# Optimization experiments

Hardware: AMD Instinct MI355X
Metric: run time of the kernel (lower is better)

## Reference

```python
import jax, jax.numpy as jnp
import numpy as np

N_NODES = 50000
N_EDGES = 600000
NODE_DIM = 64
EDGE_DIM = 16
HIDDEN = 128
N_LAYERS = 3
N_CLASSES = 2
N_GRAPHS = 256
BN_EPS = 1e-5


def setup_inputs() -> dict:
    key = jax.random.key(0)
    ks = jax.random.split(key, 24)
    i = iter(range(24))
    def nrm(shape, scale=0.05):
        return jax.random.normal(ks[next(i)], shape, dtype=jnp.float32) * scale
    inp = {
        "x": jax.random.normal(ks[next(i)], (N_NODES, NODE_DIM), dtype=jnp.float32),
        "edge_index": jax.random.randint(ks[next(i)], (2, N_EDGES), 0, N_NODES),
        "edge_attr": jax.random.normal(ks[next(i)], (N_EDGES, EDGE_DIM), dtype=jnp.float32),
        "batch": jnp.sort(jax.random.randint(ks[next(i)], (N_NODES,), 0, N_GRAPHS)),
        # encoders
        "node_w": nrm((NODE_DIM, HIDDEN)), "node_b": jnp.zeros((HIDDEN,), jnp.float32),
        "edge_w": nrm((EDGE_DIM, HIDDEN)), "edge_b": jnp.zeros((HIDDEN,), jnp.float32),
        # per-layer GINE MLP params, stacked over layers
        "mlp_w1": nrm((N_LAYERS, HIDDEN, HIDDEN)), "mlp_b1": jnp.zeros((N_LAYERS, HIDDEN), jnp.float32),
        "mlp_w2": nrm((N_LAYERS, HIDDEN, HIDDEN)), "mlp_b2": jnp.zeros((N_LAYERS, HIDDEN), jnp.float32),
        "bn_gamma": jnp.ones((N_LAYERS, HIDDEN), jnp.float32), "bn_beta": jnp.zeros((N_LAYERS, HIDDEN), jnp.float32),
        # head
        "head_w1": nrm((HIDDEN, HIDDEN)), "head_b1": jnp.zeros((HIDDEN,), jnp.float32),
        "head_w2": nrm((HIDDEN, N_CLASSES)), "head_b2": jnp.zeros((N_CLASSES,), jnp.float32),
    }
    return inp


def _forward(x, edge_attr, node_w, node_b, edge_w, edge_b, mlp_w1, mlp_b1,
             mlp_w2, mlp_b2, bn_gamma, bn_beta, head_w1, head_b1, head_w2,
             head_b2, edge_index, batch):
    src, dst = edge_index[0], edge_index[1]
    h = x @ node_w + node_b                     # [N, H]
    ea = edge_attr @ edge_w + edge_b            # [E, H]
    for l in range(N_LAYERS):
        # GINE message: relu(x_src + edge_attr), scatter-add into dst
        msg = jax.nn.relu(h[src] + ea)          # [E, H]
        agg = jax.ops.segment_sum(msg, dst, num_segments=N_NODES)
        z = h + agg                              # (1+eps)*x + agg, eps=0
        z = jax.nn.relu(z @ mlp_w1[l] + mlp_b1[l]) @ mlp_w2[l] + mlp_b2[l]
        # BatchNorm1d over node dim (batch statistics)
        mean = jnp.mean(z, axis=0)
        var = jnp.var(z, axis=0)
        z = bn_gamma[l] * (z - mean) * jax.lax.rsqrt(var + BN_EPS) + bn_beta[l]
        h = jax.nn.relu(z)                       # dropout off (eval)
    g = jax.ops.segment_sum(h, batch, num_segments=N_GRAPHS)  # global_add_pool
    return jax.nn.relu(g @ head_w1 + head_b1) @ head_w2 + head_b2


def reference(x, edge_index, edge_attr, batch, node_w, node_b, edge_w, edge_b,
              mlp_w1, mlp_b1, mlp_w2, mlp_b2, bn_gamma, bn_beta,
              head_w1, head_b1, head_w2, head_b2):
    return _forward(x, edge_attr, node_w, node_b, edge_w, edge_b, mlp_w1,
                    mlp_b1, mlp_w2, mlp_b2, bn_gamma, bn_beta, head_w1,
                    head_b1, head_w2, head_b2, edge_index, batch)
```

## Files before the change

kernel.cpp:

```cpp
#include <hip/hip_runtime.h>

#define N_NODES_C 50000
#define N_EDGES_C 600000
#define NODE_DIM_C 64
#define EDGE_DIM_C 16
#define HID 128
#define N_GRAPHS_C 256
#define BN_EPS_C 1e-5f
#define SCAN_NBLK ((N_NODES_C + 255) / 256)

typedef short bf16x8 __attribute__((ext_vector_type(8)));
typedef float f32x4 __attribute__((ext_vector_type(4)));
typedef float f32x2 __attribute__((ext_vector_type(2)));

__device__ __forceinline__ unsigned short f2bf(float f) {
  union { float f; unsigned u; } v; v.f = f;
  unsigned r = (v.u + 0x7fffu + ((v.u >> 16) & 1u)) >> 16;
  return (unsigned short)r;
}

__device__ __forceinline__ float2 bfp2f(unsigned u) {
  union { unsigned u; float f; } lo, hi;
  lo.u = u << 16;
  hi.u = u & 0xffff0000u;
  return make_float2(lo.f, hi.f);
}

__device__ __forceinline__ float bf2f(unsigned short s) {
  union { unsigned u; float f; } v;
  v.u = ((unsigned)s) << 16;
  return v.f;
}

__device__ __forceinline__ float2 fp8p2f(unsigned short u) {
  f32x2 r = __builtin_amdgcn_cvt_pk_f32_fp8((int)(unsigned)u, false);
  return make_float2(r.x, r.y);
}

__global__ __launch_bounds__(256)
void k_x2bf(const float* __restrict__ x, unsigned short* __restrict__ xb,
            int* __restrict__ cnt, float* __restrict__ g) {
  int tid = blockIdx.x * 256 + threadIdx.x;
  size_t i = (size_t)tid * 4;
  if (i < (size_t)N_NODES_C * NODE_DIM_C) {
    float4 v = *(const float4*)&x[i];
    uint2 o;
    o.x = (unsigned)f2bf(v.x) | ((unsigned)f2bf(v.y) << 16);
    o.y = (unsigned)f2bf(v.z) | ((unsigned)f2bf(v.w) << 16);
    *(uint2*)&xb[i] = o;
  }
  if (tid < N_NODES_C) cnt[tid] = 0;
  if (tid < N_GRAPHS_C * HID) g[tid] = 0.f;
}

__global__ __launch_bounds__(256)
void k_prep_w(const float* __restrict__ w1, const float* __restrict__ w2,
              const float* __restrict__ nodew, unsigned short* __restrict__ wT) {
  int m = blockIdx.x;
  if (m < 6) {
    const float* src = (m < 3) ? (w1 + (size_t)m * HID * HID)
                               : (w2 + (size_t)(m - 3) * HID * HID);
    unsigned short* dst = wT + (size_t)m * HID * HID;
    for (int i = threadIdx.x; i < HID * HID; i += 256) {
      int n = i >> 7, k = i & 127;
      dst[n * HID + k] = f2bf(src[k * HID + n]);
    }
  } else {
    unsigned short* dst = wT + (size_t)6 * HID * HID;
    for (int i = threadIdx.x; i < HID * NODE_DIM_C; i += 256) {
      int n = i >> 6, k = i & 63;
      dst[n * NODE_DIM_C + k] = f2bf(nodew[k * HID + n]);
    }
  }
}

__global__ __launch_bounds__(256)
void k_node_mfma(const unsigned short* __restrict__ xb,
                 const unsigned short* __restrict__ nwT,
                 const float* __restrict__ bias, unsigned short* __restrict__ h) {
  const int LD = NODE_DIM_C + 8;
  __shared__ unsigned short a_lds[128 * LD];
  __shared__ unsigned short w_lds[128 * LD];
  int t = threadIdx.x;
  int row0 = blockIdx.x * 128;
  {
    int r = t >> 3, c = t & 7;
#pragma unroll
    for (int it = 0; it < 4; ++it) {
      int row = it * 32 + r;
      int grow = row0 + row;
      uint4 va = (grow < N_NODES_C)
                     ? ((const uint4*)(xb + (size_t)grow * NODE_DIM_C))[c]
                     : make_uint4(0, 0, 0, 0);
      *(uint4*)&a_lds[row * LD + c * 8] = va;
      uint4 vw = ((const uint4*)(nwT + (size_t)row * NODE_DIM_C))[c];
      *(uint4*)&w_lds[row * LD + c * 8] = vw;
    }
  }
  __syncthreads();

  int lane = t & 63;
  int w = t >> 6;
  int l15 = lane & 15;
  int q = lane >> 4;

  f32x4 acc[2][8];
#pragma unroll
  for (int rt = 0; rt < 2; ++rt)
#pragma unroll
    for (int nt = 0; nt < 8; ++nt) acc[rt][nt] = (f32x4)0.f;

#pragma unroll
  for (int kk = 0; kk < 2; ++kk) {
    int k0 = kk * 32;
    bf16x8 af[2];
#pragma unroll
    for (int rt = 0; rt < 2; ++rt) {
      int arow = w * 32 + rt * 16 + l15;
      af[rt] = *(const bf16x8*)&a_lds[arow * LD + k0 + q * 8];
    }
#pragma unroll
    for (int nt = 0; nt < 8; ++nt) {
      bf16x8 bf = *(const bf16x8*)&w_lds[(nt * 16 + l15) * LD + k0 + q * 8];
#pragma unroll
      for (int rt = 0; rt < 2; ++rt)
        acc[rt][nt] = __builtin_amdgcn_mfma_f32_16x16x32_bf16(af[rt], bf, acc[rt][nt], 0, 0, 0);
    }
  }

#pragma unroll
  for (int nt = 0; nt < 8; ++nt) {
    int gcol = nt * 16 + l15;
    float bv = bias[gcol];
#pragma unroll
    for (int rt = 0; rt < 2; ++rt) {
#pragma unroll
      for (int i = 0; i < 4; ++i) {
        int grow = row0 + w * 32 + rt * 16 + q * 4 + i;
        if (grow < N_NODES_C) h[(size_t)grow * HID + gcol] = f2bf(acc[rt][nt][i] + bv);
      }
    }
  }
}

__global__ __launch_bounds__(256)
void k_histogram(const int* __restrict__ dst, int* __restrict__ counts) {
  int e = blockIdx.x * 256 + threadIdx.x;
  if (e < N_EDGES_C) atomicAdd(&counts[dst[e]], 1);
}

__global__ __launch_bounds__(256)
void k_blocksum(const int* __restrict__ cnt, int* __restrict__ partial) {
  __shared__ int ls[4];
  int t = threadIdx.x;
  int i = blockIdx.x * 256 + t;
  int v = (i < N_NODES_C) ? cnt[i] : 0;
#pragma unroll
  for (int o = 32; o > 0; o >>= 1) v += __shfl_down(v, o, 64);
  if ((t & 63) == 0) ls[t >> 6] = v;
  __syncthreads();
  if (t == 0) partial[blockIdx.x] = ls[0] + ls[1] + ls[2] + ls[3];
}

__global__ __launch_bounds__(256)
void k_scanpartials(const int* __restrict__ partial, int* __restrict__ partial_off) {
  __shared__ int s[256];
  int t = threadIdx.x;
  int v = (t < SCAN_NBLK) ? partial[t] : 0;
  s[t] = v;
  __syncthreads();
  for (int d = 1; d < 256; d <<= 1) {
    int x = (t >= d) ? s[t - d] : 0;
    __syncthreads();
    s[t] += x;
    __syncthreads();
  }
  if (t < SCAN_NBLK) partial_off[t] = s[t] - v;
}

__global__ __launch_bounds__(256)
void k_apply(int* __restrict__ cnt_cursor, const int* __restrict__ partial_off,
             int* __restrict__ row_ptr) {
  __shared__ int s[256];
  int t = threadIdx.x;
  int i = blockIdx.x * 256 + t;
  int v = (i < N_NODES_C) ? cnt_cursor[i] : 0;
  s[t] = v;
  __syncthreads();
  for (int d = 1; d < 256; d <<= 1) {
    int x = (t >= d) ? s[t - d] : 0;
    __syncthreads();
    s[t] += x;
    __syncthreads();
  }
  int excl = s[t] - v + partial_off[blockIdx.x];
  if (i < N_NODES_C) {
    row_ptr[i] = excl;
    cnt_cursor[i] = excl;
  }
  if (i == 0) row_ptr[N_NODES_C] = N_EDGES_C;
}

__global__ __launch_bounds__(256)
void k_bucket(const int* __restrict__ dst, const int* __restrict__ srcArr,
              int* __restrict__ cursor, int2* __restrict__ edata) {
  int e = blockIdx.x * 256 + threadIdx.x;
  if (e < N_EDGES_C) {
    int d = dst[e];
    int s = srcArr[e];
    int p = atomicAdd(&cursor[d], 1);
    edata[p] = make_int2(e, s);
  }
}

#define EE_LDW 40
#define EE_OSW 132
__global__ __launch_bounds__(256)
void k_edge_encode(const int2* __restrict__ edata, const float* __restrict__ eattr,
                   const float* __restrict__ ew, const float* __restrict__ ebias,
                   unsigned char* __restrict__ ea8, int* __restrict__ src_perm) {
  __shared__ unsigned short smem[128 * EE_OSW];
  unsigned short* a_lds = smem;
  unsigned short* w_lds = smem + 128 * EE_LDW;
  int t = threadIdx.x;
  int EB = blockIdx.x * 128;

  if (t < 128) {
    unsigned short tmp[16];
#pragma unroll
    for (int k = 0; k < 16; ++k) tmp[k] = f2bf(ew[k * HID + t]);
    uint4* wr = (uint4*)&w_lds[t * EE_LDW];
    wr[0] = *(uint4*)&tmp[0];
    wr[1] = *(uint4*)&tmp[8];
    wr[2] = make_uint4(0, 0, 0, 0);
    wr[3] = make_uint4(0, 0, 0, 0);
  }
  {
    int edge = t >> 1, half = t & 1;
    int gi = EB + edge;
    float4 v0 = make_float4(0, 0, 0, 0), v1 = v0;
    if (gi < N_EDGES_C) {
      int2 ed = edata[gi];
      if (half == 0) src_perm[gi] = ed.y;
      const float4* p = (const float4*)(eattr + (size_t)ed.x * EDGE_DIM_C + half * 8);
      v0 = p[0];
      v1 = p[1];
    }
    unsigned short tmp[8] = {f2bf(v0.x), f2bf(v0.y), f2bf(v0.z), f2bf(v0.w),
                             f2bf(v1.x), f2bf(v1.y), f2bf(v1.z), f2bf(v1.w)};
    *(uint4*)&a_lds[edge * EE_LDW + half * 8] = *(uint4*)tmp;
    *(uint4*)&a_lds[edge * EE_LDW + 16 + half * 8] = make_uint4(0, 0, 0, 0);
  }
  __syncthreads();

  int lane = t & 63;
  int w = t >> 6;
  int l15 = lane & 15;
  int q = lane >> 4;

  f32x4 acc[2][8];
  {
    bf16x8 af[2];
#pragma unroll
    for (int rt = 0; rt < 2; ++rt) {
      int arow = w * 32 + rt * 16 + l15;
      af[rt] = *(const bf16x8*)&a_lds[arow * EE_LDW + q * 8];
    }
#pragma unroll
    for (int nt = 0; nt < 8; ++nt) {
      bf16x8 bf = *(const bf16x8*)&w_lds[(nt * 16 + l15) * EE_LDW + q * 8];
#pragma unroll
      for (int rt = 0; rt < 2; ++rt)
        acc[rt][nt] = __builtin_amdgcn_mfma_f32_16x16x32_bf16(
            af[rt], bf, (f32x4)0.f, 0, 0, 0);
    }
  }
  __syncthreads();

#pragma unroll
  for (int nt = 0; nt < 8; ++nt) {
    int col = nt * 16 + l15;
    float bv = ebias[col];
#pragma unroll
    for (int rt = 0; rt < 2; ++rt) {
#pragma unroll
      for (int i = 0; i < 4; ++i) {
        int row = w * 32 + rt * 16 + q * 4 + i;
        smem[row * EE_OSW + col] = f2bf(acc[rt][nt][i] + bv);
      }
    }
  }
  __syncthreads();

  int valid = min(128, N_EDGES_C - EB);
  for (int i = t; i < valid * 32; i += 256) {
    int row = i >> 5, c = i & 31;
    uint2 v = *(const uint2*)&smem[row * EE_OSW + c * 4];
    float2 p0 = bfp2f(v.x);
    float2 p1 = bfp2f(v.y);
    int r = __builtin_amdgcn_cvt_pk_fp8_f32(p0.x, p0.y, 0, false);
    r = __builtin_amdgcn_cvt_pk_fp8_f32(p1.x, p1.y, r, true);
    *(unsigned*)&ea8[((size_t)EB + row) * 128 + c * 4] = (unsigned)r;
  }
}

__global__ __launch_bounds__(256)
void k_aggregate(const unsigned* __restrict__ h32, const unsigned char* __restrict__ ea8,
                 const int* __restrict__ src_p, const int* __restrict__ row_ptr,
                 unsigned short* __restrict__ z, float* __restrict__ gsum,
                 float* __restrict__ gsumsq) {
  int t = threadIdx.x;
  if (blockIdx.x == 0 && t < HID) { gsum[t] = 0.f; gsumsq[t] = 0.f; }
  int lane = t & 63;
  int wave = t >> 6;
  int node = blockIdx.x * 4 + wave;
  if (node >= N_NODES_C) return;
  float2 base = bfp2f(h32[(size_t)node * 64 + lane]);
  float acc0 = base.x, acc1 = base.y;
  int beg = row_ptr[node], end = row_ptr[node + 1];
  const unsigned char* eap = ea8 + lane * 2;
  int j = beg;
  for (; j + 8 <= end; j += 8) {
    int s0 = src_p[j],     s1 = src_p[j + 1], s2 = src_p[j + 2], s3 = src_p[j + 3];
    int s4 = src_p[j + 4], s5 = src_p[j + 5], s6 = src_p[j + 6], s7 = src_p[j + 7];
    unsigned g0 = h32[(size_t)s0 * 64 + lane];
    unsigned g1 = h32[(size_t)s1 * 64 + lane];
    unsigned g2 = h32[(size_t)s2 * 64 + lane];
    unsigned g3 = h32[(size_t)s3 * 64 + lane];
    unsigned g4 = h32[(size_t)s4 * 64 + lane];
    unsigned g5 = h32[(size_t)s5 * 64 + lane];
    unsigned g6 = h32[(size_t)s6 * 64 + lane];
    unsigned g7 = h32[(size_t)s7 * 64 + lane];
    unsigned short u0 = *(const unsigned short*)(eap + (size_t)j * 128);
    unsigned short u1 = *(const unsigned short*)(eap + (size_t)(j + 1) * 128);
    unsigned short u2 = *(const unsigned short*)(eap + (size_t)(j + 2) * 128);
    unsigned short u3 = *(const unsigned short*)(eap + (size_t)(j + 3) * 128);
    unsigned short u4 = *(const unsigned short*)(eap + (size_t)(j + 4) * 128);
    unsigned short u5 = *(const unsigned short*)(eap + (size_t)(j + 5) * 128);
    unsigned short u6 = *(const unsigned short*)(eap + (size_t)(j + 6) * 128);
    unsigned short u7 = *(const unsigned short*)(eap + (size_t)(j + 7) * 128);
    float2 a0 = bfp2f(g0), a1 = bfp2f(g1), a2 = bfp2f(g2), a3 = bfp2f(g3);
    float2 a4 = bfp2f(g4), a5 = bfp2f(g5), a6 = bfp2f(g6), a7 = bfp2f(g7);
    float2 e0 = fp8p2f(u0), e1 = fp8p2f(u1), e2 = fp8p2f(u2), e3 = fp8p2f(u3);
    float2 e4 = fp8p2f(u4), e5 = fp8p2f(u5), e6 = fp8p2f(u6), e7 = fp8p2f(u7);
    acc0 += fmaxf(a0.x + e0.x, 0.f) + fmaxf(a1.x + e1.x, 0.f) +
            fmaxf(a2.x + e2.x, 0.f) + fmaxf(a3.x + e3.x, 0.f) +
            fmaxf(a4.x + e4.x, 0.f) + fmaxf(a5.x + e5.x, 0.f) +
            fmaxf(a6.x + e6.x, 0.f) + fmaxf(a7.x + e7.x, 0.f);
    acc1 += fmaxf(a0.y + e0.y, 0.f) + fmaxf(a1.y + e1.y, 0.f) +
            fmaxf(a2.y + e2.y, 0.f) + fmaxf(a3.y + e3.y, 0.f) +
            fmaxf(a4.y + e4.y, 0.f) + fmaxf(a5.y + e5.y, 0.f) +
            fmaxf(a6.y + e6.y, 0.f) + fmaxf(a7.y + e7.y, 0.f);
  }
  for (; j + 4 <= end; j += 4) {
    int s0 = src_p[j], s1 = src_p[j + 1], s2 = src_p[j + 2], s3 = src_p[j + 3];
    unsigned g0 = h32[(size_t)s0 * 64 + lane];
    unsigned g1 = h32[(size_t)s1 * 64 + lane];
    unsigned g2 = h32[(size_t)s2 * 64 + lane];
    unsigned g3 = h32[(size_t)s3 * 64 + lane];
    unsigned short u0 = *(const unsigned short*)(eap + (size_t)j * 128);
    unsigned short u1 = *(const unsigned short*)(eap + (size_t)(j + 1) * 128);
    unsigned short u2 = *(const unsigned short*)(eap + (size_t)(j + 2) * 128);
    unsigned short u3 = *(const unsigned short*)(eap + (size_t)(j + 3) * 128);
    float2 a0 = bfp2f(g0), a1 = bfp2f(g1), a2 = bfp2f(g2), a3 = bfp2f(g3);
    float2 e0 = fp8p2f(u0), e1 = fp8p2f(u1), e2 = fp8p2f(u2), e3 = fp8p2f(u3);
    acc0 += fmaxf(a0.x + e0.x, 0.f) + fmaxf(a1.x + e1.x, 0.f) +
            fmaxf(a2.x + e2.x, 0.f) + fmaxf(a3.x + e3.x, 0.f);
    acc1 += fmaxf(a0.y + e0.y, 0.f) + fmaxf(a1.y + e1.y, 0.f) +
            fmaxf(a2.y + e2.y, 0.f) + fmaxf(a3.y + e3.y, 0.f);
  }
  for (; j < end; ++j) {
    int s0 = src_p[j];
    float2 a0 = bfp2f(h32[(size_t)s0 * 64 + lane]);
    float2 e0 = fp8p2f(*(const unsigned short*)(eap + (size_t)j * 128));
    acc0 += fmaxf(a0.x + e0.x, 0.f);
    acc1 += fmaxf(a0.y + e0.y, 0.f);
  }
  unsigned packed = (unsigned)f2bf(acc0) | ((unsigned)f2bf(acc1) << 16);
  *(unsigned*)&z[(size_t)node * HID + lane * 2] = packed;
}

__global__ __launch_bounds__(256)
void k_mlp_fused(const unsigned short* __restrict__ in,
                 const unsigned short* __restrict__ w1T,
                 const float* __restrict__ b1,
                 const unsigned short* __restrict__ w2T,
                 const float* __restrict__ b2,
                 unsigned short* __restrict__ outb,
                 float* __restrict__ gsum, float* __restrict__ gsumsq) {
  const int LDA = HID + 8;
  const int OS = 132;
  __shared__ unsigned short a_lds[128 * LDA];
  __shared__ unsigned short w_lds[128 * LDA];
  int t = threadIdx.x;
  int row0 = blockIdx.x * 128;
  {
    int r = t >> 4, chunk = t & 15;
#pragma unroll
    for (int it = 0; it < 8; ++it) {
      int row = it * 16 + r;
      int grow = row0 + row;
      uint4 va = (grow < N_NODES_C)
                     ? ((const uint4*)(in + (size_t)grow * HID))[chunk]
                     : make_uint4(0, 0, 0, 0);
      *(uint4*)&a_lds[row * LDA + chunk * 8] = va;
      uint4 vw = ((const uint4*)(w1T + (size_t)row * HID))[chunk];
      *(uint4*)&w_lds[row * LDA + chunk * 8] = vw;
    }
  }
  __syncthreads();

  int lane = t & 63;
  int w = t >> 6;
  int l15 = lane & 15;
  int q = lane >> 4;

  f32x4 acc[2][8];
#pragma unroll
  for (int rt = 0; rt < 2; ++rt)
#pragma unroll
    for (int nt = 0; nt < 8; ++nt) acc[rt][nt] = (f32x4)0.f;

#pragma unroll
  for (int kk = 0; kk < 4; ++kk) {
    int k0 = kk * 32;
    bf16x8 af[2];
#pragma unroll
    for (int rt = 0; rt < 2; ++rt) {
      int arow = w * 32 + rt * 16 + l15;
      af[rt] = *(const bf16x8*)&a_lds[arow * LDA + k0 + q * 8];
    }
#pragma unroll
    for (int nt = 0; nt < 8; ++nt) {
      int brow = nt * 16 + l15;
      bf16x8 bf = *(const bf16x8*)&w_lds[brow * LDA + k0 + q * 8];
#pragma unroll
      for (int rt = 0; rt < 2; ++rt)
        acc[rt][nt] = __builtin_amdgcn_mfma_f32_16x16x32_bf16(af[rt], bf, acc[rt][nt], 0, 0, 0);
    }
  }
  __syncthreads();

#pragma unroll
  for (int nt = 0; nt < 8; ++nt) {
    int col = nt * 16 + l15;
    float bv = b1[col];
#pragma unroll
    for (int rt = 0; rt < 2; ++rt) {
#pragma unroll
      for (int i = 0; i < 4; ++i) {
        int row = w * 32 + rt * 16 + q * 4 + i;
        a_lds[row * OS + col] = f2bf(fmaxf(acc[rt][nt][i] + bv, 0.f));
      }
    }
  }
  {
    int r = t >> 4, chunk = t & 15;
#pragma unroll
    for (int it = 0; it < 8; ++it) {
      int row = it * 16 + r;
      uint4 vw = ((const uint4*)(w2T + (size_t)row * HID))[chunk];
      *(uint4*)&w_lds[row * LDA + chunk * 8] = vw;
    }
  }
  __syncthreads();

#pragma unroll
  for (int rt = 0; rt < 2; ++rt)
#pragma unroll
    for (int nt = 0; nt < 8; ++nt) acc[rt][nt] = (f32x4)0.f;

#pragma unroll
  for (int kk = 0; kk < 4; ++kk) {
    int k0 = kk * 32;
    bf16x8 af[2];
#pragma unroll
    for (int rt = 0; rt < 2; ++rt) {
      int arow = w * 32 + rt * 16 + l15;
      af[rt] = *(const bf16x8*)&a_lds[arow * OS + k0 + q * 8];
    }
#pragma unroll
    for (int nt = 0; nt < 8; ++nt) {
      int brow = nt * 16 + l15;
      bf16x8 bf = *(const bf16x8*)&w_lds[brow * LDA + k0 + q * 8];
#pragma unroll
      for (int rt = 0; rt < 2; ++rt)
        acc[rt][nt] = __builtin_amdgcn_mfma_f32_16x16x32_bf16(af[rt], bf, acc[rt][nt], 0, 0, 0);
    }
  }

  float sp[8], qp[8];
#pragma unroll
  for (int nt = 0; nt < 8; ++nt) { sp[nt] = 0.f; qp[nt] = 0.f; }

#pragma unroll
  for (int nt = 0; nt < 8; ++nt) {
    int gcol = nt * 16 + l15;
    float bv = b2[gcol];
#pragma unroll
    for (int rt = 0; rt < 2; ++rt) {
#pragma unroll
      for (int i = 0; i < 4; ++i) {
        int grow = row0 + w * 32 + rt * 16 + q * 4 + i;
        bool ok = (grow < N_NODES_C);
        float v = acc[rt][nt][i] + bv;
        if (ok) outb[(size_t)grow * HID + gcol] = f2bf(v);
        float c = ok ? v : 0.f;
        sp[nt] += c;
        qp[nt] += c * c;
      }
    }
  }

  __syncthreads();
  float* sred = (float*)a_lds;
  float* qred = sred + 128 * 16;
  int slot = w * 4 + q;
#pragma unroll
  for (int nt = 0; nt < 8; ++nt) {
    int gcol = nt * 16 + l15;
    sred[gcol * 16 + slot] = sp[nt];
    qred[gcol * 16 + slot] = qp[nt];
  }
  __syncthreads();
  if (t < 128) {
    float s = 0.f;
#pragma unroll
    for (int i = 0; i < 16; ++i) s += sred[t * 16 + i];
    atomicAdd(&gsum[t], s);
  } else {
    int f = t - 128;
    float s = 0.f;
#pragma unroll
    for (int i = 0; i < 16; ++i) s += qred[f * 16 + i];
    atomicAdd(&gsumsq[f], s);
  }
}

__global__ __launch_bounds__(256)
void k_bn_relu(const unsigned short* __restrict__ t2, const float* __restrict__ gsum,
               const float* __restrict__ gsumsq, const float* __restrict__ gamma,
               const float* __restrict__ beta, unsigned short* __restrict__ h) {
  __shared__ float sc[HID], sh[HID];
  int t = threadIdx.x;
  if (t < HID) {
    float mean = gsum[t] * (1.f / N_NODES_C);
    float var = gsumsq[t] * (1.f / N_NODES_C) - mean * mean;
    float inv = rsqrtf(var + BN_EPS_C);
    float s = gamma[t] * inv;
    sc[t] = s;
    sh[t] = beta[t] - mean * s;
  }
  __syncthreads();
  size_t idx = ((size_t)blockIdx.x * 256 + t) * 8;
  if (idx < (size_t)N_NODES_C * HID) {
    uint4 v = *(const uint4*)&t2[idx];
    int f = (int)(idx & 127);
    float2 p0 = bfp2f(v.x), p1 = bfp2f(v.y), p2 = bfp2f(v.z), p3 = bfp2f(v.w);
    float r0 = fmaxf(p0.x * sc[f + 0] + sh[f + 0], 0.f);
    float r1 = fmaxf(p0.y * sc[f + 1] + sh[f + 1], 0.f);
    float r2 = fmaxf(p1.x * sc[f + 2] + sh[f + 2], 0.f);
    float r3 = fmaxf(p1.y * sc[f + 3] + sh[f + 3], 0.f);
    float r4 = fmaxf(p2.x * sc[f + 4] + sh[f + 4], 0.f);
    float r5 = fmaxf(p2.y * sc[f + 5] + sh[f + 5], 0.f);
    float r6 = fmaxf(p3.x * sc[f + 6] + sh[f + 6], 0.f);
    float r7 = fmaxf(p3.y * sc[f + 7] + sh[f + 7], 0.f);
    uint4 o;
    o.x = (unsigned)f2bf(r0) | ((unsigned)f2bf(r1) << 16);
    o.y = (unsigned)f2bf(r2) | ((unsigned)f2bf(r3) << 16);
    o.z = (unsigned)f2bf(r4) | ((unsigned)f2bf(r5) << 16);
    o.w = (unsigned)f2bf(r6) | ((unsigned)f2bf(r7) << 16);
    *(uint4*)&h[idx] = o;
  }
}

__global__ __launch_bounds__(128)
void k_bn_relu_pool(const unsigned short* __restrict__ t2, const float* __restrict__ gsum,
                    const float* __restrict__ gsumsq, const float* __restrict__ gamma,
                    const float* __restrict__ beta, const int* __restrict__ batch,
                    float* __restrict__ g) {
  int t = threadIdx.x;
  float mean = gsum[t] * (1.f / N_NODES_C);
  float var = gsumsq[t] * (1.f / N_NODES_C) - mean * mean;
  float inv = rsqrtf(var + BN_EPS_C);
  float sc = gamma[t] * inv;
  float sh = beta[t] - mean * sc;
  int n0 = blockIdx.x * 64;
  if (n0 >= N_NODES_C) return;
  int end = min(n0 + 64, N_NODES_C);
  int cur = batch[n0];
  float acc = 0.f;
  for (int n = n0; n < end; ++n) {
    int b = batch[n];
    if (b != cur) {
      atomicAdd(&g[cur * HID + t], acc);
      acc = 0.f;
      cur = b;
    }
    acc += fmaxf(bf2f(t2[(size_t)n * HID + t]) * sc + sh, 0.f);
  }
  atomicAdd(&g[cur * HID + t], acc);
}

__global__ __launch_bounds__(128)
void k_head(const float* __restrict__ g, const float* __restrict__ w1,
            const float* __restrict__ b1, const float* __restrict__ w2,
            const float* __restrict__ b2, float* __restrict__ out) {
  __shared__ float gs[HID];
  __shared__ float red[HID * 2];
  int gi = blockIdx.x, t = threadIdx.x;
  gs[t] = g[gi * HID + t];
  __syncthreads();
  float acc = b1[t];
#pragma unroll 8
  for (int k = 0; k < HID; ++k) acc += gs[k] * w1[k * HID + t];
  float hid = fmaxf(acc, 0.f);
  red[t * 2] = hid * w2[t * 2];
  red[t * 2 + 1] = hid * w2[t * 2 + 1];
  __syncthreads();
  for (int s = 64; s > 0; s >>= 1) {
    if (t < s) { red[t * 2] += red[(t + s) * 2]; red[t * 2 + 1] += red[(t + s) * 2 + 1]; }
    __syncthreads();
  }
  if (t == 0) {
    out[gi * 2] = red[0] + b2[0];
    out[gi * 2 + 1] = red[1] + b2[1];
  }
}

extern "C" void kernel_launch(void* const* d_in, const int* in_sizes, int n_in,
                              void* d_out, int out_size, void* d_ws, size_t ws_size,
                              hipStream_t stream) {
  const float* x      = (const float*)d_in[0];
  const int*   eidx   = (const int*)d_in[1];
  const float* eattr  = (const float*)d_in[2];
  const int*   batch  = (const int*)d_in[3];
  const float* node_w = (const float*)d_in[4];
  const float* node_b = (const float*)d_in[5];
  const float* edge_w = (const float*)d_in[6];
  const float* edge_b = (const float*)d_in[7];
  const float* mlp_w1 = (const float*)d_in[8];
  const float* mlp_b1 = (const float*)d_in[9];
  const float* mlp_w2 = (const float*)d_in[10];
  const float* mlp_b2 = (const float*)d_in[11];
  const float* bn_g   = (const float*)d_in[12];
  const float* bn_b   = (const float*)d_in[13];
  const float* hw1    = (const float*)d_in[14];
  const float* hb1    = (const float*)d_in[15];
  const float* hw2    = (const float*)d_in[16];
  const float* hb2    = (const float*)d_in[17];
  const int* srcArr = eidx;
  const int* dstArr = eidx + N_EDGES_C;

  char* wsp = (char*)d_ws;
  size_t off = 0;
  auto alloc = [&](size_t bytes) {
    void* p = wsp + off;
    off += (bytes + 255) & ~(size_t)255;
    return p;
  };
  unsigned short* h    = (unsigned short*)alloc((size_t)N_NODES_C * HID * 2);
  unsigned short* zbf  = (unsigned short*)alloc((size_t)N_NODES_C * HID * 2);
  unsigned short* t2bf = (unsigned short*)alloc((size_t)N_NODES_C * HID * 2);
  unsigned char* ea8   = (unsigned char*)alloc((size_t)N_EDGES_C * HID);
  unsigned short* xb   = (unsigned short*)alloc((size_t)N_NODES_C * NODE_DIM_C * 2);
  unsigned short* wT   = (unsigned short*)alloc(((size_t)6 * HID * HID + HID * NODE_DIM_C) * 2);
  int* row_ptr   = (int*)alloc((N_NODES_C + 1) * 4);
  int* cnt_cur   = (int*)alloc(N_NODES_C * 4);
  int2* edata    = (int2*)alloc((size_t)N_EDGES_C * 8);
  int* src_perm  = (int*)alloc((size_t)N_EDGES_C * 4);
  int* partial   = (int*)alloc(256 * 4);
  int* partial_off = (int*)alloc(256 * 4);
  float* gsum    = (float*)alloc(HID * 4);
  float* gsumsq  = (float*)alloc(HID * 4);
  float* g       = (float*)alloc((size_t)N_GRAPHS_C * HID * 4);
  unsigned short* nwT = wT + (size_t)6 * HID * HID;

  k_x2bf<<<(N_NODES_C * NODE_DIM_C / 4 + 255) / 256, 256, 0, stream>>>(x, xb,
                                                                       cnt_cur, g);
  k_prep_w<<<7, 256, 0, stream>>>(mlp_w1, mlp_w2, node_w, wT);
  k_node_mfma<<<(N_NODES_C + 127) / 128, 256, 0, stream>>>(xb, nwT, node_b, h);
  k_histogram<<<(N_EDGES_C + 255) / 256, 256, 0, stream>>>(dstArr, cnt_cur);
  k_blocksum<<<SCAN_NBLK, 256, 0, stream>>>(cnt_cur, partial);
  k_scanpartials<<<1, 256, 0, stream>>>(partial, partial_off);
  k_apply<<<SCAN_NBLK, 256, 0, stream>>>(cnt_cur, partial_off, row_ptr);
  k_bucket<<<(N_EDGES_C + 255) / 256, 256, 0, stream>>>(dstArr, srcArr, cnt_cur,
                                                        edata);
  k_edge_encode<<<(N_EDGES_C + 127) / 128, 256, 0, stream>>>(edata, eattr, edge_w,
                                                             edge_b, ea8, src_perm);

  const int GB = (N_NODES_C + 127) / 128;
  for (int l = 0; l < 3; ++l) {
    k_aggregate<<<(N_NODES_C + 3) / 4, 256, 0, stream>>>((const unsigned*)h, ea8,
                                                         src_perm, row_ptr, zbf,
                                                         gsum, gsumsq);
    k_mlp_fused<<<GB, 256, 0, stream>>>(
        zbf, wT + (size_t)l * HID * HID, mlp_b1 + l * HID,
        wT + (size_t)(3 + l) * HID * HID, mlp_b2 + l * HID, t2bf, gsum, gsumsq);
    if (l < 2) {
      k_bn_relu<<<(N_NODES_C * HID / 8 + 255) / 256, 256, 0, stream>>>(
          t2bf, gsum, gsumsq, bn_g + l * HID, bn_b + l * HID, h);
    } else {
      k_bn_relu_pool<<<(N_NODES_C + 63) / 64, 128, 0, stream>>>(
          t2bf, gsum, gsumsq, bn_g + l * HID, bn_b + l * HID, batch, g);
    }
  }
  k_head<<<N_GRAPHS_C, 128, 0, stream>>>(g, hw1, hb1, hw2, hb2, (float*)d_out);
}
```

Baseline: 479.6 us.

## Fuse BatchNorm+ReLU into next layer's gather, replace elementwise pass with finalize

The standalone BN+ReLU kernel, which read and wrote the whole 50000x128 bf16 activation tensor, is removed for layers 0 and 1. A tiny one-block kernel now computes the per-feature scale and shift and resets the statistics accumulators. The next aggregate kernel applies scale, shift and ReLU on the fly to each gathered neighbour row and to its own row. This saves a full read-write pass per layer, but repeats the affine+ReLU about 12 times per node inside the gather, adding ALU work to a memory-bound loop.

```diff
diff --git a/kernel.cpp b/kernel.cpp
--- a/kernel.cpp
+++ b/kernel.cpp
@@ -39,7 +39,8 @@
 
 __global__ __launch_bounds__(256)
 void k_x2bf(const float* __restrict__ x, unsigned short* __restrict__ xb,
-            int* __restrict__ cnt, float* __restrict__ g) {
+            int* __restrict__ cnt, float* __restrict__ g,
+            float* __restrict__ gsum, float* __restrict__ gsumsq) {
   int tid = blockIdx.x * 256 + threadIdx.x;
   size_t i = (size_t)tid * 4;
   if (i < (size_t)N_NODES_C * NODE_DIM_C) {
@@ -51,6 +52,7 @@
   }
   if (tid < N_NODES_C) cnt[tid] = 0;
   if (tid < N_GRAPHS_C * HID) g[tid] = 0.f;
+  if (tid < HID) { gsum[tid] = 0.f; gsumsq[tid] = 0.f; }
 }
 
 __global__ __launch_bounds__(256)
@@ -304,18 +306,30 @@
   }
 }
 
-__global__ __launch_bounds__(256)
-void k_aggregate(const unsigned* __restrict__ h32, const unsigned char* __restrict__ ea8,
+template <bool ACT>
+__global__ __launch_bounds__(256)
+void k_aggregate(const unsigned* __restrict__ in32, const unsigned char* __restrict__ ea8,
                  const int* __restrict__ src_p, const int* __restrict__ row_ptr,
-                 unsigned short* __restrict__ z, float* __restrict__ gsum,
-                 float* __restrict__ gsumsq) {
+                 const float* __restrict__ scb, const float* __restrict__ shb,
+                 unsigned short* __restrict__ z) {
   int t = threadIdx.x;
-  if (blockIdx.x == 0 && t < HID) { gsum[t] = 0.f; gsumsq[t] = 0.f; }
   int lane = t & 63;
   int wave = t >> 6;
   int node = blockIdx.x * 4 + wave;
   if (node >= N_NODES_C) return;
-  float2 base = bfp2f(h32[(size_t)node * 64 + lane]);
+  float sc0 = 1.f, sc1 = 1.f, sh0 = 0.f, sh1 = 0.f;
+  if constexpr (ACT) {
+    int f0 = lane * 2;
+    sc0 = scb[f0]; sc1 = scb[f0 + 1];
+    sh0 = shb[f0]; sh1 = shb[f0 + 1];
+  }
+  auto act = [&](float2 p) -> float2 {
+    if constexpr (ACT)
+      return make_float2(fmaxf(p.x * sc0 + sh0, 0.f), fmaxf(p.y * sc1 + sh1, 0.f));
+    else
+      return p;
+  };
+  float2 base = act(bfp2f(in32[(size_t)node * 64 + lane]));
   float acc0 = base.x, acc1 = base.y;
   int beg = row_ptr[node], end = row_ptr[node + 1];
   const unsigned char* eap = ea8 + lane * 2;
@@ -323,14 +337,14 @@
   for (; j + 8 <= end; j += 8) {
     int s0 = src_p[j],     s1 = src_p[j + 1], s2 = src_p[j + 2], s3 = src_p[j + 3];
     int s4 = src_p[j + 4], s5 = src_p[j + 5], s6 = src_p[j + 6], s7 = src_p[j + 7];
-    unsigned g0 = h32[(size_t)s0 * 64 + lane];
-    unsigned g1 = h32[(size_t)s1 * 64 + lane];
-    unsigned g2 = h32[(size_t)s2 * 64 + lane];
-    unsigned g3 = h32[(size_t)s3 * 64 + lane];
-    unsigned g4 = h32[(size_t)s4 * 64 + lane];
-    unsigned g5 = h32[(size_t)s5 * 64 + lane];
-    unsigned g6 = h32[(size_t)s6 * 64 + lane];
-    unsigned g7 = h32[(size_t)s7 * 64 + lane];
+    unsigned g0 = in32[(size_t)s0 * 64 + lane];
+    unsigned g1 = in32[(size_t)s1 * 64 + lane];
+    unsigned g2 = in32[(size_t)s2 * 64 + lane];
+    unsigned g3 = in32[(size_t)s3 * 64 + lane];
+    unsigned g4 = in32[(size_t)s4 * 64 + lane];
+    unsigned g5 = in32[(size_t)s5 * 64 + lane];
+    unsigned g6 = in32[(size_t)s6 * 64 + lane];
+    unsigned g7 = in32[(size_t)s7 * 64 + lane];
     unsigned short u0 = *(const unsigned short*)(eap + (size_t)j * 128);
     unsigned short u1 = *(const unsigned short*)(eap + (size_t)(j + 1) * 128);
     unsigned short u2 = *(const unsigned short*)(eap + (size_t)(j + 2) * 128);
@@ -339,8 +353,8 @@
     unsigned short u5 = *(const unsigned short*)(eap + (size_t)(j + 5) * 128);
     unsigned short u6 = *(const unsigned short*)(eap + (size_t)(j + 6) * 128);
     unsigned short u7 = *(const unsigned short*)(eap + (size_t)(j + 7) * 128);
-    float2 a0 = bfp2f(g0), a1 = bfp2f(g1), a2 = bfp2f(g2), a3 = bfp2f(g3);
-    float2 a4 = bfp2f(g4), a5 = bfp2f(g5), a6 = bfp2f(g6), a7 = bfp2f(g7);
+    float2 a0 = act(bfp2f(g0)), a1 = act(bfp2f(g1)), a2 = act(bfp2f(g2)), a3 = act(bfp2f(g3));
+    float2 a4 = act(bfp2f(g4)), a5 = act(bfp2f(g5)), a6 = act(bfp2f(g6)), a7 = act(bfp2f(g7));
     float2 e0 = fp8p2f(u0), e1 = fp8p2f(u1), e2 = fp8p2f(u2), e3 = fp8p2f(u3);
     float2 e4 = fp8p2f(u4), e5 = fp8p2f(u5), e6 = fp8p2f(u6), e7 = fp8p2f(u7);
     acc0 += fmaxf(a0.x + e0.x, 0.f) + fmaxf(a1.x + e1.x, 0.f) +
@@ -354,15 +368,15 @@
   }
   for (; j + 4 <= end; j += 4) {
     int s0 = src_p[j], s1 = src_p[j + 1], s2 = src_p[j + 2], s3 = src_p[j + 3];
-    unsigned g0 = h32[(size_t)s0 * 64 + lane];
-    unsigned g1 = h32[(size_t)s1 * 64 + lane];
-    unsigned g2 = h32[(size_t)s2 * 64 + lane];
-    unsigned g3 = h32[(size_t)s3 * 64 + lane];
+    unsigned g0 = in32[(size_t)s0 * 64 + lane];
+    unsigned g1 = in32[(size_t)s1 * 64 + lane];
+    unsigned g2 = in32[(size_t)s2 * 64 + lane];
+    unsigned g3 = in32[(size_t)s3 * 64 + lane];
     unsigned short u0 = *(const unsigned short*)(eap + (size_t)j * 128);
     unsigned short u1 = *(const unsigned short*)(eap + (size_t)(j + 1) * 128);
     unsigned short u2 = *(const unsigned short*)(eap + (size_t)(j + 2) * 128);
     unsigned short u3 = *(const unsigned short*)(eap + (size_t)(j + 3) * 128);
-    float2 a0 = bfp2f(g0), a1 = bfp2f(g1), a2 = bfp2f(g2), a3 = bfp2f(g3);
+    float2 a0 = act(bfp2f(g0)), a1 = act(bfp2f(g1)), a2 = act(bfp2f(g2)), a3 = act(bfp2f(g3));
     float2 e0 = fp8p2f(u0), e1 = fp8p2f(u1), e2 = fp8p2f(u2), e3 = fp8p2f(u3);
     acc0 += fmaxf(a0.x + e0.x, 0.f) + fmaxf(a1.x + e1.x, 0.f) +
             fmaxf(a2.x + e2.x, 0.f) + fmaxf(a3.x + e3.x, 0.f);
@@ -371,7 +385,7 @@
   }
   for (; j < end; ++j) {
     int s0 = src_p[j];
-    float2 a0 = bfp2f(h32[(size_t)s0 * 64 + lane]);
+    float2 a0 = act(bfp2f(in32[(size_t)s0 * 64 + lane]));
     float2 e0 = fp8p2f(*(const unsigned short*)(eap + (size_t)j * 128));
     acc0 += fmaxf(a0.x + e0.x, 0.f);
     acc1 += fmaxf(a0.y + e0.y, 0.f);
@@ -537,41 +551,18 @@
   }
 }
 
-__global__ __launch_bounds__(256)
-void k_bn_relu(const unsigned short* __restrict__ t2, const float* __restrict__ gsum,
-               const float* __restrict__ gsumsq, const float* __restrict__ gamma,
-               const float* __restrict__ beta, unsigned short* __restrict__ h) {
-  __shared__ float sc[HID], sh[HID];
-  int t = threadIdx.x;
-  if (t < HID) {
-    float mean = gsum[t] * (1.f / N_NODES_C);
-    float var = gsumsq[t] * (1.f / N_NODES_C) - mean * mean;
-    float inv = rsqrtf(var + BN_EPS_C);
-    float s = gamma[t] * inv;
-    sc[t] = s;
-    sh[t] = beta[t] - mean * s;
-  }
-  __syncthreads();
-  size_t idx = ((size_t)blockIdx.x * 256 + t) * 8;
-  if (idx < (size_t)N_NODES_C * HID) {
-    uint4 v = *(const uint4*)&t2[idx];
-    int f = (int)(idx & 127);
-    float2 p0 = bfp2f(v.x), p1 = bfp2f(v.y), p2 = bfp2f(v.z), p3 = bfp2f(v.w);
-    float r0 = fmaxf(p0.x * sc[f + 0] + sh[f + 0], 0.f);
-    float r1 = fmaxf(p0.y * sc[f + 1] + sh[f + 1], 0.f);
-    float r2 = fmaxf(p1.x * sc[f + 2] + sh[f + 2], 0.f);
-    float r3 = fmaxf(p1.y * sc[f + 3] + sh[f + 3], 0.f);
-    float r4 = fmaxf(p2.x * sc[f + 4] + sh[f + 4], 0.f);
-    float r5 = fmaxf(p2.y * sc[f + 5] + sh[f + 5], 0.f);
-    float r6 = fmaxf(p3.x * sc[f + 6] + sh[f + 6], 0.f);
-    float r7 = fmaxf(p3.y * sc[f + 7] + sh[f + 7], 0.f);
-    uint4 o;
-    o.x = (unsigned)f2bf(r0) | ((unsigned)f2bf(r1) << 16);
-    o.y = (unsigned)f2bf(r2) | ((unsigned)f2bf(r3) << 16);
-    o.z = (unsigned)f2bf(r4) | ((unsigned)f2bf(r5) << 16);
-    o.w = (unsigned)f2bf(r6) | ((unsigned)f2bf(r7) << 16);
-    *(uint4*)&h[idx] = o;
-  }
+__global__ void k_bn_finalize(float* __restrict__ gsum, float* __restrict__ gsumsq,
+                              const float* __restrict__ gamma, const float* __restrict__ beta,
+                              float* __restrict__ scb, float* __restrict__ shb) {
+  int f = threadIdx.x;
+  float mean = gsum[f] * (1.f / N_NODES_C);
+  float var = gsumsq[f] * (1.f / N_NODES_C) - mean * mean;
+  float inv = rsqrtf(var + BN_EPS_C);
+  float sc = gamma[f] * inv;
+  scb[f] = sc;
+  shb[f] = beta[f] - mean * sc;
+  gsum[f] = 0.f;
+  gsumsq[f] = 0.f;
 }
 
 __global__ __launch_bounds__(128)
@@ -673,11 +664,13 @@
   int* partial_off = (int*)alloc(256 * 4);
   float* gsum    = (float*)alloc(HID * 4);
   float* gsumsq  = (float*)alloc(HID * 4);
+  float* scb     = (float*)alloc(HID * 4);
+  float* shb     = (float*)alloc(HID * 4);
   float* g       = (float*)alloc((size_t)N_GRAPHS_C * HID * 4);
   unsigned short* nwT = wT + (size_t)6 * HID * HID;
 
-  k_x2bf<<<(N_NODES_C * NODE_DIM_C / 4 + 255) / 256, 256, 0, stream>>>(x, xb,
-                                                                       cnt_cur, g);
+  k_x2bf<<<(N_NODES_C * NODE_DIM_C / 4 + 255) / 256, 256, 0, stream>>>(
+      x, xb, cnt_cur, g, gsum, gsumsq);
   k_prep_w<<<7, 256, 0, stream>>>(mlp_w1, mlp_w2, node_w, wT);
   k_node_mfma<<<(N_NODES_C + 127) / 128, 256, 0, stream>>>(xb, nwT, node_b, h);
   k_histogram<<<(N_EDGES_C + 255) / 256, 256, 0, stream>>>(dstArr, cnt_cur);
@@ -690,16 +683,21 @@
                                                              edge_b, ea8, src_perm);
 
   const int GB = (N_NODES_C + 127) / 128;
+  const int AB = (N_NODES_C + 3) / 4;
   for (int l = 0; l < 3; ++l) {
-    k_aggregate<<<(N_NODES_C + 3) / 4, 256, 0, stream>>>((const unsigned*)h, ea8,
-                                                         src_perm, row_ptr, zbf,
-                                                         gsum, gsumsq);
+    if (l == 0) {
+      k_aggregate<false><<<AB, 256, 0, stream>>>((const unsigned*)h, ea8, src_perm,
+                                                 row_ptr, nullptr, nullptr, zbf);
+    } else {
+      k_aggregate<true><<<AB, 256, 0, stream>>>((const unsigned*)t2bf, ea8, src_perm,
+                                                row_ptr, scb, shb, zbf);
+    }
     k_mlp_fused<<<GB, 256, 0, stream>>>(
         zbf, wT + (size_t)l * HID * HID, mlp_b1 + l * HID,
         wT + (size_t)(3 + l) * HID * HID, mlp_b2 + l * HID, t2bf, gsum, gsumsq);
     if (l < 2) {
-      k_bn_relu<<<(N_NODES_C * HID / 8 + 255) / 256, 256, 0, stream>>>(
-          t2bf, gsum, gsumsq, bn_g + l * HID, bn_b + l * HID, h);
+      k_bn_finalize<<<1, HID, 0, stream>>>(gsum, gsumsq, bn_g + l * HID,
+                                           bn_b + l * HID, scb, shb);
     } else {
       k_bn_relu_pool<<<(N_NODES_C + 63) / 64, 128, 0, stream>>>(
           t2bf, gsum, gsumsq, bn_g + l * HID, bn_b + l * HID, batch, g);
```

New measurement: 469.2 us. -2.2%, faster.
